# Kernel optimization log

Hardware: AMD Instinct MI355X
Metric: run time of the kernel (lower is better)

## Reference

```python
import jax, jax.numpy as jnp
import numpy as np

TEMPERATURE = 0.1
WEIGHT = 5.0
IS_SYMMETRIC = True


def setup_inputs() -> dict:
    key = jax.random.key(0)
    k1, k2, k3, k4, k5 = jax.random.split(key, 5)
    B, D = 2048, 128
    z_hat = jax.random.normal(k1, (1, B, D), dtype=jnp.float32)  # unused except batch size
    mu_x = jax.random.normal(k2, (B, D), dtype=jnp.float32)
    sigma_x = jax.random.uniform(k3, (B, D), minval=0.5, maxval=1.5, dtype=jnp.float32)
    mu_p = jax.random.normal(k4, (B, D), dtype=jnp.float32)
    sigma_p = jax.random.uniform(k5, (B, D), minval=0.5, maxval=1.5, dtype=jnp.float32)
    return {"z_hat": z_hat, "mu_x": mu_x, "sigma_x": sigma_x, "mu_p": mu_p, "sigma_p": sigma_p}


def _pairwise_kl(mus, sigmas):
    # K[a, b] = KL( N(mu_b, sig_b) || N(mu_a, sig_a) )  (matches torch repeat/repeat_interleave layout)
    D = mus.shape[1]
    var = sigmas * sigmas                      # [N, D]
    inv = 1.0 / var                            # [N, D]
    logdet = jnp.sum(jnp.log(sigmas), axis=1)  # [N]
    tr = jnp.einsum("ad,bd->ab", inv, var)                       # sum_d var_b / var_a
    quad = (jnp.einsum("ad,bd->ab", inv, mus * mus)
            - 2.0 * jnp.einsum("ad,bd->ab", mus * inv, mus)
            + jnp.sum(mus * mus * inv, axis=1)[:, None])         # sum_d (mu_b - mu_a)^2 / var_a
    return logdet[:, None] - logdet[None, :] + 0.5 * (tr + quad) - 0.5 * D


def reference(z_hat, mu_x, sigma_x, mu_p, sigma_p):
    B = mu_x.shape[0]
    N = 2 * B
    mus = jnp.concatenate([mu_x, mu_p], axis=0)       # [N, D]
    sigmas = jnp.concatenate([sigma_x, sigma_p], axis=0)

    logits = -_pairwise_kl(mus, sigmas)               # [N, N]
    if IS_SYMMETRIC:
        logits = (logits + logits.T) / 2
    logits = logits / TEMPERATURE

    # is_invariant=True: drop the diagonal -> [N, N-1] (static gather, jit-friendly)
    rows = jnp.arange(N)[:, None]
    cols = jnp.arange(N - 1)[None, :]
    idx = cols + (cols >= rows).astype(cols.dtype)    # skip column == row
    logits = jnp.take_along_axis(logits, jnp.broadcast_to(idx, (N, N - 1)), axis=1)

    n_classes = N - 1
    ar = jnp.arange(B)
    pos_idx = jnp.concatenate([ar + B - 1, ar], axis=0)  # [N]

    # weight != 1 branch: add -log(to_mult) at the positive logit of each row
    to_mult = (n_classes - 1.0 / WEIGHT) / (n_classes - 1)
    to_add = -jnp.log(jnp.asarray(to_mult, logits.dtype))
    logits = logits.at[jnp.arange(N), pos_idx].add(to_add)

    logp = jax.nn.log_softmax(logits, axis=1)
    hat_H_mlz = -jnp.mean(logp[jnp.arange(N), pos_idx])
    return hat_H_mlz
```

## Files before the change

### kernel.cpp

```cpp
#include <hip/hip_runtime.h>
#include <hip/hip_bf16.h>
#include <math.h>

typedef short bf16x8 __attribute__((ext_vector_type(8)));
typedef float f32x4 __attribute__((ext_vector_type(4)));

#define B_HALF 2048
#define N_TOT  4096
#define D_DIM  128
#define K_DIM  512
#define NGRP   32
#define NBLK   528
#define KSTEPS 16

__device__ unsigned red_done;

__global__ __launch_bounds__(256) void prep_feat(
    const float* __restrict__ mu_x, const float* __restrict__ sigma_x,
    const float* __restrict__ mu_p, const float* __restrict__ sigma_p,
    __hip_bfloat16* __restrict__ Gf, float* __restrict__ a) {
  const int tid = threadIdx.x;
  const int wv = tid >> 6;
  const int ln = tid & 63;
  const int d0 = ln * 2;
  const float SQ2 = 1.41421356237309515f;
#pragma unroll
  for (int rr = 0; rr < 16; rr += 4) {
    const int row = blockIdx.x * 16 + rr + wv;
    const float* mup = (row < B_HALF) ? mu_x : mu_p;
    const float* sgp = (row < B_HALF) ? sigma_x : sigma_p;
    const int gi = row & (B_HALF - 1);
    const float2 m2 = *(const float2*)(mup + gi * D_DIM + d0);
    const float2 s2 = *(const float2*)(sgp + gi * D_DIM + d0);
    float var0 = s2.x * s2.x, inv0 = 1.0f / var0, vm0 = var0 + m2.x * m2.x;
    float var1 = s2.y * s2.y, inv1 = 1.0f / var1, vm1 = var1 + m2.y * m2.y;
    size_t base = (size_t)row * K_DIM;
    __hip_bfloat162 h;
    unsigned ub;
#define PK2(OFF, X, Y)                                                        \
    h.x = __float2bfloat16(X); h.y = __float2bfloat16(Y);                     \
    __builtin_memcpy(&ub, &h, 4);                                             \
    __builtin_nontemporal_store(ub, (unsigned*)(Gf + base + (OFF) + d0));
    PK2(0,   inv0, inv1)
    PK2(128, vm0, vm1)
    PK2(256, SQ2 * m2.x * inv0, SQ2 * m2.y * inv1)
    PK2(384, -SQ2 * m2.x, -SQ2 * m2.y)
#undef PK2
    float av = m2.x * m2.x * inv0 + m2.y * m2.y * inv1;
#pragma unroll
    for (int x = 1; x < 64; x <<= 1) av += __shfl_xor(av, x);
    if (ln == 0) __builtin_nontemporal_store(av, &a[row]);
  }
}

#define GLOAD16(src, dst)                                                     \
  __builtin_amdgcn_global_load_lds(                                           \
      (const __attribute__((address_space(1))) void*)(src),                   \
      (__attribute__((address_space(3))) void*)(dst), 16, 0, 0)

__global__ __launch_bounds__(256, 3) void gemm_lse(
    const __hip_bfloat16* __restrict__ Gf, const float* __restrict__ a,
    float* __restrict__ lsep, float* __restrict__ pos, float to_add) {
  __shared__ char lt[3][128 * 64];
  __shared__ char rt[3][128 * 64];
  __shared__ float2 red[128][2];

  const int sb = (blockIdx.x & 7) * (NBLK / 8) + (blockIdx.x >> 3);
  int rb, cb;
  if (sb < 144) {
    const int k = sb / 36;
    int t = sb - k * 36;
    int i = 0;
    while (t >= 8 - i) { t -= 8 - i; ++i; }
    rb = k * 8 + i;
    cb = k * 8 + i + t;
  } else {
    const int o = (sb - 144) >> 6;
    const int t = (sb - 144) & 63;
    const int k1 = (o < 3) ? 0 : ((o < 5) ? 1 : 2);
    const int k2 = (o < 3) ? (o + 1) : ((o < 5) ? (o - 1) : 3);
    rb = k1 * 8 + (t >> 3);
    cb = k2 * 8 + (t & 7);
  }

  const int tid  = threadIdx.x;
  const int lane = tid & 63;
  const int wave = tid >> 6;
  const int rowBase = rb * 128, colBase = cb * 128;
  const int wr = wave >> 1, wc = wave & 1;
  const int lx = lane & 15;
  const int rq = lane >> 4;

  f32x4 acc[4][4];
#pragma unroll
  for (int m = 0; m < 4; ++m)
#pragma unroll
    for (int n = 0; n < 4; ++n) acc[m][n] = (f32x4){0.f, 0.f, 0.f, 0.f};

  const int sr  = lane >> 2;
  const int scb = (((lane & 3) ^ (sr & 3)) << 4);
  const char* lsrc0 = (const char*)Gf + (size_t)rowBase * (K_DIM * 2);
  const char* rsrc0 = (const char*)Gf + (size_t)colBase * (K_DIM * 2);

#define STAGE(KK)                                                             \
  {                                                                           \
    const int b_ = (KK) % 3;                                                  \
    const char* ls_ = lsrc0 + (KK) * 64;                                      \
    const char* rs_ = rsrc0 + ((KK) ^ 4) * 64;                                \
    _Pragma("unroll")                                                         \
    for (int g = 0; g < 2; ++g) {                                             \
      const int row_ = wave * 32 + g * 16;                                    \
      GLOAD16(ls_ + (size_t)(row_ + sr) * 1024 + scb, &lt[b_][row_ * 64]);    \
      GLOAD16(rs_ + (size_t)(row_ + sr) * 1024 + scb, &rt[b_][row_ * 64]);    \
    }                                                                         \
  }

  STAGE(0)
  STAGE(1)

#pragma unroll
  for (int kk = 0; kk < KSTEPS; ++kk) {
    if (kk < KSTEPS - 1) asm volatile("s_waitcnt vmcnt(4)" ::: "memory");
    else                 asm volatile("s_waitcnt vmcnt(0)" ::: "memory");
    __builtin_amdgcn_s_barrier();
    __builtin_amdgcn_sched_barrier(0);
    if (kk + 2 < KSTEPS) STAGE(kk + 2)
    const int b = kk % 3;
    bf16x8 af[4], bg[4];
    const int kbp = ((rq ^ (lx & 3)) << 4);
#pragma unroll
    for (int m = 0; m < 4; ++m) {
      const int row = wr * 64 + m * 16 + lx;
      af[m] = *(const bf16x8*)(&lt[b][row * 64 + kbp]);
    }
#pragma unroll
    for (int n = 0; n < 4; ++n) {
      const int row = wc * 64 + n * 16 + lx;
      bg[n] = *(const bf16x8*)(&rt[b][row * 64 + kbp]);
    }
#pragma unroll
    for (int m = 0; m < 4; ++m)
#pragma unroll
      for (int n = 0; n < 4; ++n)
        acc[m][n] = __builtin_amdgcn_mfma_f32_16x16x32_bf16(af[m], bg[n], acc[m][n], 0, 0, 0);
  }
#undef STAGE

  const float c0 = 640.0f;
  const float c1 = 2.5f;
  float aR[4][4];
#pragma unroll
  for (int m = 0; m < 4; ++m)
#pragma unroll
    for (int v = 0; v < 4; ++v)
      aR[m][v] = a[rowBase + wr * 64 + m * 16 + rq * 4 + v];
  float aC[4];
#pragma unroll
  for (int n = 0; n < 4; ++n) aC[n] = a[colBase + wc * 64 + n * 16 + lx];

#pragma unroll
  for (int m = 0; m < 4; ++m)
#pragma unroll
    for (int n = 0; n < 4; ++n)
#pragma unroll
      for (int v = 0; v < 4; ++v) {
        int grow = rowBase + wr * 64 + m * 16 + rq * 4 + v;
        int gcol = colBase + wc * 64 + n * 16 + lx;
        float S = c0 - c1 * (acc[m][n][v] + aR[m][v] + aC[n]);
        if (gcol == grow) {
          S = -INFINITY;
        } else if (gcol == (grow ^ B_HALF)) {
          S += to_add;
          __builtin_nontemporal_store(S, &pos[grow]);
          __builtin_nontemporal_store(S, &pos[gcol]);
        }
        acc[m][n][v] = S;
      }

#pragma unroll
  for (int m = 0; m < 4; ++m)
#pragma unroll
    for (int v = 0; v < 4; ++v) {
      float pm = -INFINITY;
#pragma unroll
      for (int n = 0; n < 4; ++n) pm = fmaxf(pm, acc[m][n][v]);
#pragma unroll
      for (int x = 1; x < 16; x <<= 1) pm = fmaxf(pm, __shfl_xor(pm, x));
      float ps = 0.f;
#pragma unroll
      for (int n = 0; n < 4; ++n) ps += __expf(acc[m][n][v] - pm);
#pragma unroll
      for (int x = 1; x < 16; x <<= 1) ps += __shfl_xor(ps, x);
      if (lx == 0) red[wr * 64 + m * 16 + rq * 4 + v][wc] = make_float2(pm, ps);
    }
  __syncthreads();
  if (tid < 128) {
    float2 p0 = red[tid][0], p1 = red[tid][1];
    float M = fmaxf(p0.x, p1.x);
    float S = p0.y * __expf(p0.x - M) + p1.y * __expf(p1.x - M);
    __builtin_nontemporal_store(M + logf(S),
                                &lsep[(size_t)(rowBase + tid) * NGRP + cb]);
  }

  if (rb != cb) {
    __syncthreads();
#pragma unroll
    for (int n = 0; n < 4; ++n) {
      float cm = -INFINITY;
#pragma unroll
      for (int m = 0; m < 4; ++m)
#pragma unroll
        for (int v = 0; v < 4; ++v) cm = fmaxf(cm, acc[m][n][v]);
      cm = fmaxf(cm, __shfl_xor(cm, 16));
      cm = fmaxf(cm, __shfl_xor(cm, 32));
      float cs = 0.f;
#pragma unroll
      for (int m = 0; m < 4; ++m)
#pragma unroll
        for (int v = 0; v < 4; ++v) cs += __expf(acc[m][n][v] - cm);
      cs += __shfl_xor(cs, 16);
      cs += __shfl_xor(cs, 32);
      if (lane < 16) red[wc * 64 + n * 16 + lane][wr] = make_float2(cm, cs);
    }
    __syncthreads();
    if (tid < 128) {
      float2 p0 = red[tid][0], p1 = red[tid][1];
      float M = fmaxf(p0.x, p1.x);
      float S = p0.y * __expf(p0.x - M) + p1.y * __expf(p1.x - M);
      __builtin_nontemporal_store(M + logf(S),
                                  &lsep[(size_t)(colBase + tid) * NGRP + rb]);
    }
  }
}

__global__ __launch_bounds__(256) void reduce_final(
    const float* __restrict__ lsep, const float* __restrict__ pos,
    float* __restrict__ partial, float* __restrict__ out) {
  const int tid = threadIdx.x;
  const int row = blockIdx.x * 256 + tid;
  const float* lp = lsep + (size_t)row * NGRP;
  float M = lp[0];
#pragma unroll
  for (int k = 1; k < NGRP; ++k) M = fmaxf(M, lp[k]);
  float s = 0.f;
#pragma unroll
  for (int k = 0; k < NGRP; ++k) s += __expf(lp[k] - M);
  float contrib = (M + logf(s)) - pos[row];

  __shared__ float fr[256];
  fr[tid] = contrib;
  __syncthreads();
#pragma unroll
  for (int off = 128; off > 0; off >>= 1) {
    if (tid < off) fr[tid] += fr[tid + off];
    __syncthreads();
  }
  if (tid == 0) {
    partial[blockIdx.x] = fr[0];
    unsigned v = __hip_atomic_fetch_add(&red_done, 1u, __ATOMIC_ACQ_REL,
                                        __HIP_MEMORY_SCOPE_AGENT);
    if (v == 15u) {
      float tot = 0.f;
      for (int k = 0; k < 16; ++k) tot += partial[k];
      out[0] = tot * (1.0f / 4096.0f);
      __hip_atomic_store(&red_done, 0u, __ATOMIC_RELAXED,
                         __HIP_MEMORY_SCOPE_AGENT);
    }
  }
}

extern "C" void kernel_launch(void* const* d_in, const int* in_sizes, int n_in,
                              void* d_out, int out_size, void* d_ws, size_t ws_size,
                              hipStream_t stream) {
  const float* mu_x    = (const float*)d_in[1];
  const float* sigma_x = (const float*)d_in[2];
  const float* mu_p    = (const float*)d_in[3];
  const float* sigma_p = (const float*)d_in[4];
  float* out = (float*)d_out;

  float to_add = (float)(-log((4095.0 - 1.0 / 5.0) / 4094.0));

  const size_t featB = (size_t)N_TOT * K_DIM * 2;
  char* ws = (char*)d_ws;
  __hip_bfloat16* Gf = (__hip_bfloat16*)(ws);
  float* a       = (float*)(ws + featB);
  float* lsep    = (float*)(ws + featB + 16384);
  float* pos     = (float*)(ws + featB + 16384 + 524288);
  float* partial = (float*)(ws + featB + 16384 + 524288 + 16384);

  prep_feat<<<dim3(256), dim3(256), 0, stream>>>(mu_x, sigma_x, mu_p, sigma_p,
                                                 Gf, a);
  gemm_lse<<<dim3(NBLK), dim3(256), 0, stream>>>(Gf, a, lsep, pos, to_add);
  reduce_final<<<dim3(16), dim3(256), 0, stream>>>(lsep, pos, partial, out);
}
```

Measured before the change: 39.54 us.

## Switch pairwise KL GEMM features from bf16 to fp8 MFMA

```diff
diff --git a/kernel.cpp b/kernel.cpp
--- a/kernel.cpp
+++ b/kernel.cpp
@@ -2,23 +2,27 @@
 #include <hip/hip_bf16.h>
 #include <math.h>
 
-typedef short bf16x8 __attribute__((ext_vector_type(8)));
 typedef float f32x4 __attribute__((ext_vector_type(4)));
+typedef long  i64;
 
 #define B_HALF 2048
 #define N_TOT  4096
 #define D_DIM  128
-#define K_DIM  512
 #define NGRP   32
 #define NBLK   528
-#define KSTEPS 16
+#define KSTEPS 8
+#define ROWB   512
 
 __device__ unsigned red_done;
+
+__device__ __forceinline__ short pk8(float x, float y) {
+  return (short)__builtin_amdgcn_cvt_pk_fp8_f32(x, y, 0, false);
+}
 
 __global__ __launch_bounds__(256) void prep_feat(
     const float* __restrict__ mu_x, const float* __restrict__ sigma_x,
     const float* __restrict__ mu_p, const float* __restrict__ sigma_p,
-    __hip_bfloat16* __restrict__ Gf, float* __restrict__ a) {
+    unsigned char* __restrict__ Gf8, float* __restrict__ a) {
   const int tid = threadIdx.x;
   const int wv = tid >> 6;
   const int ln = tid & 63;
@@ -34,22 +38,16 @@
     const float2 s2 = *(const float2*)(sgp + gi * D_DIM + d0);
     float var0 = s2.x * s2.x, inv0 = 1.0f / var0, vm0 = var0 + m2.x * m2.x;
     float var1 = s2.y * s2.y, inv1 = 1.0f / var1, vm1 = var1 + m2.y * m2.y;
-    size_t base = (size_t)row * K_DIM;
-    __hip_bfloat162 h;
-    unsigned ub;
-#define PK2(OFF, X, Y)                                                        \
-    h.x = __float2bfloat16(X); h.y = __float2bfloat16(Y);                     \
-    __builtin_memcpy(&ub, &h, 4);                                             \
-    __builtin_nontemporal_store(ub, (unsigned*)(Gf + base + (OFF) + d0));
-    PK2(0,   inv0, inv1)
-    PK2(128, vm0, vm1)
-    PK2(256, SQ2 * m2.x * inv0, SQ2 * m2.y * inv1)
-    PK2(384, -SQ2 * m2.x, -SQ2 * m2.y)
-#undef PK2
+    size_t base = (size_t)row * ROWB;
+    *(short*)(Gf8 + base + 0   + d0) = pk8(inv0, inv1);
+    *(short*)(Gf8 + base + 128 + d0) = pk8(vm0, vm1);
+    *(short*)(Gf8 + base + 256 + d0) = pk8(SQ2 * m2.x * inv0, SQ2 * m2.y * inv1);
+    *(short*)(Gf8 + base + 384 + d0) = pk8(-SQ2 * m2.x, -SQ2 * m2.y);
+
     float av = m2.x * m2.x * inv0 + m2.y * m2.y * inv1;
 #pragma unroll
     for (int x = 1; x < 64; x <<= 1) av += __shfl_xor(av, x);
-    if (ln == 0) __builtin_nontemporal_store(av, &a[row]);
+    if (ln == 0) a[row] = av;
   }
 }
 
@@ -59,7 +57,7 @@
       (__attribute__((address_space(3))) void*)(dst), 16, 0, 0)
 
 __global__ __launch_bounds__(256, 3) void gemm_lse(
-    const __hip_bfloat16* __restrict__ Gf, const float* __restrict__ a,
+    const unsigned char* __restrict__ Gf8, const float* __restrict__ a,
     float* __restrict__ lsep, float* __restrict__ pos, float to_add) {
   __shared__ char lt[3][128 * 64];
   __shared__ char rt[3][128 * 64];
@@ -99,19 +97,19 @@
 
   const int sr  = lane >> 2;
   const int scb = (((lane & 3) ^ (sr & 3)) << 4);
-  const char* lsrc0 = (const char*)Gf + (size_t)rowBase * (K_DIM * 2);
-  const char* rsrc0 = (const char*)Gf + (size_t)colBase * (K_DIM * 2);
+  const char* lsrc0 = (const char*)Gf8 + (size_t)rowBase * ROWB;
+  const char* rsrc0 = (const char*)Gf8 + (size_t)colBase * ROWB;
 
 #define STAGE(KK)                                                             \
   {                                                                           \
     const int b_ = (KK) % 3;                                                  \
     const char* ls_ = lsrc0 + (KK) * 64;                                      \
-    const char* rs_ = rsrc0 + ((KK) ^ 4) * 64;                                \
+    const char* rs_ = rsrc0 + ((KK) ^ 2) * 64;                                \
     _Pragma("unroll")                                                         \
     for (int g = 0; g < 2; ++g) {                                             \
       const int row_ = wave * 32 + g * 16;                                    \
-      GLOAD16(ls_ + (size_t)(row_ + sr) * 1024 + scb, &lt[b_][row_ * 64]);    \
-      GLOAD16(rs_ + (size_t)(row_ + sr) * 1024 + scb, &rt[b_][row_ * 64]);    \
+      GLOAD16(ls_ + (size_t)(row_ + sr) * ROWB + scb, &lt[b_][row_ * 64]);    \
+      GLOAD16(rs_ + (size_t)(row_ + sr) * ROWB + scb, &rt[b_][row_ * 64]);    \
     }                                                                         \
   }
 
@@ -126,23 +124,27 @@
     __builtin_amdgcn_sched_barrier(0);
     if (kk + 2 < KSTEPS) STAGE(kk + 2)
     const int b = kk % 3;
-    bf16x8 af[4], bg[4];
-    const int kbp = ((rq ^ (lx & 3)) << 4);
-#pragma unroll
-    for (int m = 0; m < 4; ++m) {
-      const int row = wr * 64 + m * 16 + lx;
-      af[m] = *(const bf16x8*)(&lt[b][row * 64 + kbp]);
-    }
-#pragma unroll
-    for (int n = 0; n < 4; ++n) {
-      const int row = wc * 64 + n * 16 + lx;
-      bg[n] = *(const bf16x8*)(&rt[b][row * 64 + kbp]);
-    }
-#pragma unroll
-    for (int m = 0; m < 4; ++m)
-#pragma unroll
-      for (int n = 0; n < 4; ++n)
-        acc[m][n] = __builtin_amdgcn_mfma_f32_16x16x32_bf16(af[m], bg[n], acc[m][n], 0, 0, 0);
+#pragma unroll
+    for (int ks = 0; ks < 2; ++ks) {
+      i64 af[4], bg[4];
+      const int q16 = ks * 2 + (rq >> 1);
+      const int sub = (rq & 1) * 8;
+#pragma unroll
+      for (int m = 0; m < 4; ++m) {
+        const int row = wr * 64 + m * 16 + lx;
+        af[m] = *(const i64*)(&lt[b][row * 64 + ((q16 ^ (row & 3)) << 4) + sub]);
+      }
+#pragma unroll
+      for (int n = 0; n < 4; ++n) {
+        const int row = wc * 64 + n * 16 + lx;
+        bg[n] = *(const i64*)(&rt[b][row * 64 + ((q16 ^ (row & 3)) << 4) + sub]);
+      }
+#pragma unroll
+      for (int m = 0; m < 4; ++m)
+#pragma unroll
+        for (int n = 0; n < 4; ++n)
+          acc[m][n] = __builtin_amdgcn_mfma_f32_16x16x32_fp8_fp8(af[m], bg[n], acc[m][n], 0, 0, 0);
+    }
   }
 #undef STAGE
 
@@ -171,8 +173,8 @@
           S = -INFINITY;
         } else if (gcol == (grow ^ B_HALF)) {
           S += to_add;
-          __builtin_nontemporal_store(S, &pos[grow]);
-          __builtin_nontemporal_store(S, &pos[gcol]);
+          pos[grow] = S;
+          pos[gcol] = S;
         }
         acc[m][n][v] = S;
       }
@@ -198,8 +200,7 @@
     float2 p0 = red[tid][0], p1 = red[tid][1];
     float M = fmaxf(p0.x, p1.x);
     float S = p0.y * __expf(p0.x - M) + p1.y * __expf(p1.x - M);
-    __builtin_nontemporal_store(M + logf(S),
-                                &lsep[(size_t)(rowBase + tid) * NGRP + cb]);
+    lsep[(size_t)(rowBase + tid) * NGRP + cb] = M + logf(S);
   }
 
   if (rb != cb) {
@@ -227,8 +228,7 @@
       float2 p0 = red[tid][0], p1 = red[tid][1];
       float M = fmaxf(p0.x, p1.x);
       float S = p0.y * __expf(p0.x - M) + p1.y * __expf(p1.x - M);
-      __builtin_nontemporal_store(M + logf(S),
-                                  &lsep[(size_t)(colBase + tid) * NGRP + rb]);
+      lsep[(size_t)(colBase + tid) * NGRP + rb] = M + logf(S);
     }
   }
 }
@@ -280,16 +280,16 @@
 
   float to_add = (float)(-log((4095.0 - 1.0 / 5.0) / 4094.0));
 
-  const size_t featB = (size_t)N_TOT * K_DIM * 2;
+  const size_t featB = (size_t)N_TOT * ROWB;
   char* ws = (char*)d_ws;
-  __hip_bfloat16* Gf = (__hip_bfloat16*)(ws);
+  unsigned char* Gf8 = (unsigned char*)(ws);
   float* a       = (float*)(ws + featB);
   float* lsep    = (float*)(ws + featB + 16384);
   float* pos     = (float*)(ws + featB + 16384 + 524288);
   float* partial = (float*)(ws + featB + 16384 + 524288 + 16384);
 
   prep_feat<<<dim3(256), dim3(256), 0, stream>>>(mu_x, sigma_x, mu_p, sigma_p,
-                                                 Gf, a);
-  gemm_lse<<<dim3(NBLK), dim3(256), 0, stream>>>(Gf, a, lsep, pos, to_add);
+                                                 Gf8, a);
+  gemm_lse<<<dim3(NBLK), dim3(256), 0, stream>>>(Gf8, a, lsep, pos, to_add);
   reduce_final<<<dim3(16), dim3(256), 0, stream>>>(lsep, pos, partial, out);
 }
```

Result: faster. 37.15 us, median of 2 (-6.0%).
